# Kernel optimization log

Measured on AMD Instinct MI355X. Metric: run time of the kernel, lower is better.

Reference implementation:

```python
import jax, jax.numpy as jnp
import numpy as np

# Module hyperparameters (from init_kwargs)
DG = 8          # deformable_groups
KH = KW = 3     # kernel size
STRIDE = 1
PAD = 1
DIL = 1


def conv2d(x, w, b):
    # x: [B,C,H,W], w: [O,I,kh,kw] -> [B,O,Ho,Wo]
    y = jax.lax.conv_general_dilated(
        x, w, window_strides=(STRIDE, STRIDE),
        padding=[(PAD, PAD), (PAD, PAD)],
        rhs_dilation=(DIL, DIL),
        dimension_numbers=('NCHW', 'OIHW', 'NCHW'))
    return y + b[None, :, None, None]


def deform_conv2d(inp, offset, mask, w, b):
    # torchvision.ops.DeformConv2d (v2, with modulation mask), groups=1.
    # offset: [B, 2*DG*K, Ho, Wo] laid out as (dg, k, (dy,dx));
    # mask:   [B, DG*K, Ho, Wo] (already sigmoided).
    B, C, H, W = inp.shape
    Cout = w.shape[0]
    K = KH * KW
    Ho, Wo = offset.shape[2], offset.shape[3]
    Cg = C // DG

    off = offset.reshape(B, DG, K, 2, Ho, Wo)
    # base sampling grid per kernel tap
    ky = jnp.repeat(jnp.arange(KH) * DIL, KW)        # [K]
    kx = jnp.tile(jnp.arange(KW) * DIL, KH)          # [K]
    ybase = jnp.arange(Ho) * STRIDE - PAD            # [Ho]
    xbase = jnp.arange(Wo) * STRIDE - PAD            # [Wo]
    ys = off[:, :, :, 0] + (ky[:, None, None] + ybase[None, :, None])  # [B,DG,K,Ho,Wo]
    xs = off[:, :, :, 1] + (kx[:, None, None] + xbase[None, None, :])

    y0 = jnp.floor(ys)
    x0 = jnp.floor(xs)
    wy = (ys - y0)[:, :, None]   # [B,DG,1,K,Ho,Wo]
    wx = (xs - x0)[:, :, None]
    y0i = y0.astype(jnp.int32)
    x0i = x0.astype(jnp.int32)

    flat = inp.reshape(B, DG, Cg, H * W)

    def gather(yi, xi):
        valid = (yi >= 0) & (yi < H) & (xi >= 0) & (xi < W)        # [B,DG,K,Ho,Wo]
        idx = jnp.clip(yi, 0, H - 1) * W + jnp.clip(xi, 0, W - 1)
        idxf = idx.reshape(B, DG, -1)
        g = jax.vmap(jax.vmap(lambda f, i: jnp.take(f, i, axis=1)))(flat, idxf)
        g = g.reshape(B, DG, Cg, K, Ho, Wo)
        return g * valid[:, :, None].astype(inp.dtype)

    v00 = gather(y0i, x0i)
    v01 = gather(y0i, x0i + 1)
    v10 = gather(y0i + 1, x0i)
    v11 = gather(y0i + 1, x0i + 1)
    val = (v00 * (1 - wy) * (1 - wx) + v01 * (1 - wy) * wx
           + v10 * wy * (1 - wx) + v11 * wy * wx)
    val = val * mask.reshape(B, DG, 1, K, Ho, Wo)
    val = val.reshape(B, C, K, Ho, Wo)
    out = jnp.einsum('bckhw,ock->bohw', val, w.reshape(Cout, C, K))
    return out + b[None, :, None, None]


def setup_inputs() -> dict:
    key = jax.random.key(0)
    ks = jax.random.split(key, 8)
    B, C, Cf, Cout, H, W = 4, 64, 64, 64, 128, 128
    K = KH * KW
    inp = jax.random.normal(ks[0], (B, C, H, W), jnp.float32)
    feature = jax.random.normal(ks[1], (B, Cf, H, W), jnp.float32)
    # conv_offset / conv_mask params (small init so sampled offsets stay local)
    w_off = 0.05 * jax.random.normal(ks[2], (2 * DG * K, Cf, KH, KW), jnp.float32)
    b_off = jnp.zeros((2 * DG * K,), jnp.float32)
    w_mask = 0.05 * jax.random.normal(ks[3], (DG * K, Cf, KH, KW), jnp.float32)
    b_mask = jnp.zeros((DG * K,), jnp.float32)
    # deform conv params
    fan_in = C * KH * KW
    w_dcn = jax.random.normal(ks[4], (Cout, C, KH, KW), jnp.float32) / np.sqrt(fan_in)
    b_dcn = 0.01 * jax.random.normal(ks[5], (Cout,), jnp.float32)
    return {"input": inp, "feature": feature,
            "w_off": w_off, "b_off": b_off,
            "w_mask": w_mask, "b_mask": b_mask,
            "w_dcn": w_dcn, "b_dcn": b_dcn}


def reference(input, feature, w_off, b_off, w_mask, b_mask, w_dcn, b_dcn):
    offset = conv2d(feature, w_off, b_off)
    mask = jax.nn.sigmoid(conv2d(feature, w_mask, b_mask))
    return deform_conv2d(input, offset, mask, w_dcn, b_dcn)
```

## Files before the change

### kernel.cpp

```cpp
#include <hip/hip_runtime.h>
#include <hip/hip_bf16.h>

#define NB 4
#define CIN 64
#define COUT 64
#define HH 128
#define WW 128
#define HW (HH*WW)
#define C_OFF 144
#define C_OM 216
#define C_PAD 224
#define KTOT 576

typedef __attribute__((ext_vector_type(8))) short bf16x8;
typedef __attribute__((ext_vector_type(4))) float f32x4;
typedef __attribute__((ext_vector_type(8))) unsigned short uv8;

__device__ inline unsigned short f2bf(float f) {
    union { float f; unsigned u; } v; v.f = f;
    unsigned r = (v.u + 0x7FFF + ((v.u >> 16) & 1)) >> 16;
    return (unsigned short)r;
}

__device__ inline float bf2f(unsigned short h) {
    union { unsigned u; float f; } v; v.u = ((unsigned)h) << 16; return v.f;
}


__global__ __launch_bounds__(256) void transpose_wdcn(const float* __restrict__ w,
                                                      float* __restrict__ wT) {
    int idx = blockIdx.x * 256 + threadIdx.x;
    if (idx < KTOT * COUT) {
        int o = idx & 63, kk = idx >> 6;
        wT[idx] = w[o * KTOT + kk];
    }
}

__global__ __launch_bounds__(256) void to_nhwc_bf16_2(const float* __restrict__ f0,
                                                      unsigned short* __restrict__ o0,
                                                      const float* __restrict__ f1,
                                                      unsigned short* __restrict__ o1) {
    int t = blockIdx.x * 256 + threadIdx.x;
    const float* src;
    unsigned short* dst;
    int tt = t & 65535;
    int b = tt >> 14, yx = tt & 16383;
    if (t < 65536) { src = f0 + (size_t)b * CIN * HW + yx; dst = o0 + (size_t)tt * 64; }
    else           { src = f1 + (size_t)b * CIN * HW + yx; dst = o1 + (size_t)tt * 64; }
#pragma unroll
    for (int c8 = 0; c8 < 8; ++c8) {
        uv8 v;
#pragma unroll
        for (int j = 0; j < 8; ++j) v[j] = f2bf(src[(size_t)(c8 * 8 + j) * HW]);
        *(uv8*)(dst + c8 * 8) = v;
    }
}

__global__ __launch_bounds__(256) void prep_weights(const float* __restrict__ w_off,
                                                    const float* __restrict__ w_mask,
                                                    const float* __restrict__ w_dcn,
                                                    unsigned short* __restrict__ wB,
                                                    unsigned short* __restrict__ wTf2) {
    int idx = blockIdx.x * 256 + threadIdx.x;
    if (idx < C_PAD * KTOT) {
        int co = idx / KTOT, k = idx - co * KTOT;
        int t = k >> 6, ci = k & 63;
        float v = 0.f;
        if (co < C_OFF)      v = w_off[(size_t)co * KTOT + ci * 9 + t];
        else if (co < C_OM)  v = w_mask[(size_t)(co - C_OFF) * KTOT + ci * 9 + t];
        wB[idx] = f2bf(v);
    } else if (idx < C_PAD * KTOT + 72 * 64 * 8) {
        int j = idx - C_PAD * KTOT;
        int q = j >> 9;
        int co = (j >> 3) & 63;
        int r = j & 7;
        int k = q >> 3, dg = q & 7;
        wTf2[j] = f2bf(w_dcn[(size_t)co * KTOT + (dg * 8 + r) * 9 + k]);
    }
}


__global__ __launch_bounds__(256, 4) void dcn_fused(
    const unsigned short* __restrict__ fnhwc,
    const unsigned short* __restrict__ inb,
    const unsigned short* __restrict__ wB,
    const unsigned short* __restrict__ wTf2,
    const float* __restrict__ b_off, const float* __restrict__ b_mask,
    const float* __restrict__ b_dcn,
    float* __restrict__ out)
{
    __shared__ __align__(16) unsigned char smem[36864];
    unsigned short* Ash0  = (unsigned short*)smem;
    unsigned short* Ash1  = (unsigned short*)(smem + 4096);
    unsigned short* Bsh   = (unsigned short*)(smem + 8192);
    float* om_l           = (float*)smem;
    unsigned short* val_q = (unsigned short*)smem;

    int tid = threadIdx.x;
    int bid = blockIdx.x;
    int b   = bid >> 8;
    int hw0 = (bid & 255) << 6;
    int ho  = hw0 >> 7;
    int wo0 = hw0 & 127;

    int lane = tid & 63, wave = tid >> 6;
    int arow = lane & 15, g = lane >> 4;
    int h  = wave & 1;
    int ws = wave >> 1;

    f32x4 acc0[7], acc1[7];
#pragma unroll
    for (int n = 0; n < 7; ++n) {
        acc0[n] = (f32x4){0.f, 0.f, 0.f, 0.f};
        acc1[n] = (f32x4){0.f, 0.f, 0.f, 0.f};
    }

    int px_w = tid >> 3;
    int c8_w = tid & 7;
    const uv8 zero8 = (uv8){0, 0, 0, 0, 0, 0, 0, 0};

    for (int t = 0; t < 9; ++t) {
        int ky = t / 3, kx = t - ky * 3;
        int y = ho + ky - 1;
        bool yv = (unsigned)y < (unsigned)HH;
        __syncthreads();
#pragma unroll
        for (int pt = 0; pt < 2; ++pt) {
            int x = wo0 + pt * 32 + px_w + kx - 1;
            uv8 v = zero8;
            if (yv && (unsigned)x < (unsigned)WW)
                v = *(const uv8*)(fnhwc + ((size_t)((b * HH + y) * WW + x) << 6) + c8_w * 8);
            int off16 = (c8_w << 4) ^ ((px_w & 7) << 4);
            char* dst = (char*)(pt ? Ash1 : Ash0);
            *(uv8*)(dst + px_w * 128 + off16) = v;
        }
#pragma unroll
        for (int r = 0; r < 7; ++r) {
            int idx = r * 256 + tid;
            int co = idx >> 3, c8 = idx & 7;
            uv8 v = *(const uv8*)(wB + (size_t)co * KTOT + t * 64 + c8 * 8);
            *(uv8*)((char*)Bsh + co * 128 + ((c8 << 4) ^ ((co & 7) << 4))) = v;
        }
        __syncthreads();
#pragma unroll
        for (int half = 0; half < 2; ++half) {
            int px = h * 16 + arow;
            int kb = half * 64 + g * 16;
            bf16x8 a0 = *(const bf16x8*)((const char*)Ash0 + px * 128 + (kb ^ ((px & 7) << 4)));
            bf16x8 a1 = *(const bf16x8*)((const char*)Ash1 + px * 128 + (kb ^ ((px & 7) << 4)));
#pragma unroll
            for (int n = 0; n < 7; ++n) {
                int co = ws * 112 + n * 16 + arow;
                bf16x8 bf = *(const bf16x8*)((const char*)Bsh + co * 128 +
                                             (kb ^ ((co & 7) << 4)));
                acc0[n] = __builtin_amdgcn_mfma_f32_16x16x32_bf16(a0, bf, acc0[n], 0, 0, 0);
                acc1[n] = __builtin_amdgcn_mfma_f32_16x16x32_bf16(a1, bf, acc1[n], 0, 0, 0);
            }
        }
    }
    __syncthreads();

#pragma unroll
    for (int pt = 0; pt < 2; ++pt) {
        int hw0t = hw0 + pt * 32;
        int wo0t = wo0 + pt * 32;

#pragma unroll
        for (int n = 0; n < 7; ++n) {
            int co = ws * 112 + n * 16 + arow;
            if (co < C_OM) {
                float bias = (co < C_OFF) ? b_off[co] : b_mask[co - C_OFF];
                f32x4 av = pt ? acc1[n] : acc0[n];
#pragma unroll
                for (int j = 0; j < 4; ++j) {
                    float v = av[j] + bias;
                    if (co >= C_OFF) v = 1.f / (1.f + __expf(-v));
                    om_l[co * 33 + h * 16 + g * 4 + j] = v;
                }
            }
        }
        __syncthreads();

        int px = tid & 31;
        int dg = tid >> 5;

        float dy[9], dxv[9], mk[9];
#pragma unroll
        for (int k = 0; k < 9; ++k) {
            dy[k]  = om_l[(dg * 18 + 2 * k) * 33 + px];
            dxv[k] = om_l[(dg * 18 + 2 * k + 1) * 33 + px];
            mk[k]  = om_l[(C_OFF + dg * 9 + k) * 33 + px];
        }
        __syncthreads();

        const unsigned short* plane0 = inb + ((size_t)b * HW << 6) + dg * 8;
        float yb = (float)(ho - 1);
        float xb = (float)(wo0t + px - 1);

#pragma unroll
        for (int k = 0; k < 9; ++k) {
            float ys = dy[k] + yb + (float)(k / 3);
            float xs = dxv[k] + xb + (float)(k % 3);
            float y0f = floorf(ys), x0f = floorf(xs);
            float fy = ys - y0f, fx = xs - x0f;
            int y0 = (int)y0f, x0 = (int)x0f;
            bool yv0 = (unsigned)y0 < (unsigned)HH;
            bool yv1 = (unsigned)(y0 + 1) < (unsigned)HH;
            bool xv0 = (unsigned)x0 < (unsigned)WW;
            bool xv1 = (unsigned)(x0 + 1) < (unsigned)WW;
            const unsigned short* pp = plane0 + (y0 * WW + x0) * 64;
            uv8 c00 = zero8, c01 = zero8, c10 = zero8, c11 = zero8;
            if (yv0 && xv0) c00 = *(const uv8*)(pp);
            if (yv0 && xv1) c01 = *(const uv8*)(pp + 64);
            if (yv1 && xv0) c10 = *(const uv8*)(pp + 64 * WW);
            if (yv1 && xv1) c11 = *(const uv8*)(pp + 64 * WW + 64);
            uv8 r;
#pragma unroll
            for (int j = 0; j < 8; ++j) {
                float v00 = bf2f(c00[j]), v01 = bf2f(c01[j]);
                float v10 = bf2f(c10[j]), v11 = bf2f(c11[j]);
                float top = v00 + (v01 - v00) * fx;
                float bot = v10 + (v11 - v10) * fx;
                float v = top + (bot - top) * fy;
                r[j] = f2bf(v * mk[k]);
            }
            *(uv8*)(val_q + (k * 8 + dg) * 256 + px * 8) = r;
        }
        __syncthreads();

        int nh = wave >> 1;

        f32x4 dacc[2];
        dacc[0] = dacc[1] = (f32x4){0.f, 0.f, 0.f, 0.f};
#pragma unroll
        for (int s = 0; s < 18; ++s) {
            int q = s * 4 + g;
            bf16x8 a = *(const bf16x8*)(val_q + q * 256 + (h * 16 + arow) * 8);
#pragma unroll
            for (int n = 0; n < 2; ++n) {
                int co = nh * 32 + n * 16 + arow;
                bf16x8 bfr = *(const bf16x8*)(wTf2 + ((size_t)q * 64 + co) * 8);
                dacc[n] = __builtin_amdgcn_mfma_f32_16x16x32_bf16(a, bfr, dacc[n], 0, 0, 0);
            }
        }

#pragma unroll
        for (int n = 0; n < 2; ++n) {
            int co = nh * 32 + n * 16 + arow;
            float bias = b_dcn[co];
            f32x4 r;
#pragma unroll
            for (int j = 0; j < 4; ++j) r[j] = dacc[n][j] + bias;
            *(f32x4*)(out + (size_t)b * COUT * HW + (size_t)co * HW + hw0t + h * 16 + g * 4) = r;
        }
        __syncthreads();
    }
}


__global__ __launch_bounds__(256) void conv_om_kernel(
    const float* __restrict__ feature,
    const float* __restrict__ w_off, const float* __restrict__ b_off,
    const float* __restrict__ w_mask, const float* __restrict__ b_mask,
    float* __restrict__ om)
{
    int tid = threadIdx.x;
    int p = blockIdx.x * 256 + tid;
    int cg = blockIdx.y;
    int b  = p >> 14;
    int hw = p & (HW - 1);
    int ho = hw >> 7;
    int wo = hw & 127;
    int co0 = cg * 4;

    float acc[4];
    const float* wb[4];
#pragma unroll
    for (int j = 0; j < 4; ++j) {
        int co = co0 + j;
        if (co < C_OFF) { acc[j] = b_off[co];          wb[j] = w_off  + (size_t)co * 576; }
        else            { acc[j] = b_mask[co - C_OFF]; wb[j] = w_mask + (size_t)(co - C_OFF) * 576; }
    }
    const float* fb = feature + (size_t)b * CIN * HW;
    for (int ci = 0; ci < CIN; ++ci) {
        const float* fp = fb + ci * HW;
#pragma unroll
        for (int ky = 0; ky < 3; ++ky) {
            int y = ho + ky - 1;
            bool yvb = (unsigned)y < (unsigned)HH;
#pragma unroll
            for (int kx = 0; kx < 3; ++kx) {
                int x = wo + kx - 1;
                float v = (yvb && (unsigned)x < (unsigned)WW) ? fp[y * WW + x] : 0.f;
                int wi = ci * 9 + ky * 3 + kx;
#pragma unroll
                for (int j = 0; j < 4; ++j) acc[j] += v * wb[j][wi];
            }
        }
    }
    size_t obase = (size_t)b * C_OM * HW + hw;
#pragma unroll
    for (int j = 0; j < 4; ++j) {
        int co = co0 + j;
        float v = acc[j];
        if (co >= C_OFF) v = 1.f / (1.f + __expf(-v));
        om[obase + (size_t)co * HW] = v;
    }
}

__global__ __launch_bounds__(256) void dcn_kernel(
    const float* __restrict__ input,
    const float* __restrict__ om,
    const float* __restrict__ wT,
    const float* __restrict__ b_dcn,
    float* __restrict__ out)
{
    __shared__ float om_l[C_OM * 16];
    __shared__ float val_l[KTOT * 16];

    int tid  = threadIdx.x;
    int tile = blockIdx.x;
    int b    = tile >> 10;
    int hw0  = (tile & 1023) << 4;
    int ho   = hw0 >> 7;
    int wo0  = hw0 & 127;

    const float* omg = om + (size_t)b * C_OM * HW + hw0;
    for (int i = tid; i < C_OM * 16; i += 256) {
        int ch = i >> 4, px = i & 15;
        om_l[i] = omg[(size_t)ch * HW + px];
    }
    __syncthreads();

    for (int pair = tid; pair < 1024; pair += 256) {
        int px = pair & 15, c = pair >> 4;
        int dg = c >> 3;
        const float* plane = input + (size_t)(b * CIN + c) * HW;
        float yb = (float)(ho - 1);
        float xb = (float)(wo0 + px - 1);
#pragma unroll
        for (int k = 0; k < 9; ++k) {
            float dyv = om_l[(dg * 18 + 2 * k) * 16 + px];
            float dxv = om_l[(dg * 18 + 2 * k + 1) * 16 + px];
            float m  = om_l[(C_OFF + dg * 9 + k) * 16 + px];
            float ys = dyv + yb + (float)(k / 3);
            float xs = dxv + xb + (float)(k % 3);
            float y0f = floorf(ys), x0f = floorf(xs);
            float wy = ys - y0f, wx = xs - x0f;
            int y0 = (int)y0f, x0 = (int)x0f;
            bool yv0 = (unsigned)y0 < (unsigned)HH;
            bool yv1 = (unsigned)(y0 + 1) < (unsigned)HH;
            bool xv0 = (unsigned)x0 < (unsigned)WW;
            bool xv1 = (unsigned)(x0 + 1) < (unsigned)WW;
            const float* r0 = plane + y0 * WW + x0;
            float v00 = (yv0 && xv0) ? r0[0]      : 0.f;
            float v01 = (yv0 && xv1) ? r0[1]      : 0.f;
            float v10 = (yv1 && xv0) ? r0[WW]     : 0.f;
            float v11 = (yv1 && xv1) ? r0[WW + 1] : 0.f;
            float top = v00 + (v01 - v00) * wx;
            float bot = v10 + (v11 - v10) * wx;
            float v = top + (bot - top) * wy;
            val_l[(c * 9 + k) * 16 + px] = v * m;
        }
    }
    __syncthreads();

    int o2 = tid & 31;
    int ph = tid >> 5;
    int o0 = o2 * 2, px0 = ph * 2;
    float a00 = b_dcn[o0],     a01 = b_dcn[o0];
    float a10 = b_dcn[o0 + 1], a11 = b_dcn[o0 + 1];
    for (int kk = 0; kk < KTOT; ++kk) {
        float2 wv = *reinterpret_cast<const float2*>(wT + kk * 64 + o0);
        float va = val_l[kk * 16 + px0];
        float vb = val_l[kk * 16 + px0 + 1];
        a00 += wv.x * va; a01 += wv.x * vb;
        a10 += wv.y * va; a11 += wv.y * vb;
    }
    float* ob = out + (size_t)b * COUT * HW + hw0;
    ob[(size_t)o0 * HW + px0]           = a00;
    ob[(size_t)o0 * HW + px0 + 1]       = a01;
    ob[(size_t)(o0 + 1) * HW + px0]     = a10;
    ob[(size_t)(o0 + 1) * HW + px0 + 1] = a11;
}

extern "C" void kernel_launch(void* const* d_in, const int* in_sizes, int n_in,
                              void* d_out, int out_size, void* d_ws, size_t ws_size,
                              hipStream_t stream) {
    const float* input   = (const float*)d_in[0];
    const float* feature = (const float*)d_in[1];
    const float* w_off   = (const float*)d_in[2];
    const float* b_off   = (const float*)d_in[3];
    const float* w_mask  = (const float*)d_in[4];
    const float* b_mask  = (const float*)d_in[5];
    const float* w_dcn   = (const float*)d_in[6];
    const float* b_dcn   = (const float*)d_in[7];
    float* out = (float*)d_out;

    unsigned short* fnhwc = (unsigned short*)d_ws;
    unsigned short* wBp   = fnhwc + (size_t)NB * HW * CIN;
    unsigned short* wTfp  = wBp + (size_t)C_PAD * KTOT;
    unsigned short* inb   = wTfp + 72 * 64 * 8;
    size_t need_full = (size_t)((char*)(inb + (size_t)NB * HW * CIN) - (char*)d_ws);
    size_t need_fb = ((size_t)NB * C_OM * HW + KTOT * COUT) * sizeof(float);

    if (ws_size >= need_full) {
        to_nhwc_bf16_2<<<NB * HW * 2 / 256, 256, 0, stream>>>(feature, fnhwc, input, inb);
        prep_weights<<<(C_PAD * KTOT + 72 * 64 * 8 + 255) / 256, 256, 0, stream>>>(
            w_off, w_mask, w_dcn, wBp, wTfp);
        dcn_fused<<<NB * HW / 64, 256, 0, stream>>>(fnhwc, inb, wBp, wTfp,
                                                    b_off, b_mask, b_dcn, out);
    } else if (ws_size >= need_fb) {
        float* om = (float*)d_ws;
        float* wT = om + (size_t)NB * C_OM * HW;
        transpose_wdcn<<<(KTOT * COUT + 255) / 256, 256, 0, stream>>>(w_dcn, wT);
        dim3 cgrid(NB * HW / 256, 54);
        conv_om_kernel<<<cgrid, 256, 0, stream>>>(feature, w_off, b_off, w_mask, b_mask, om);
        dcn_kernel<<<NB * HW / 16, 256, 0, stream>>>(input, om, wT, b_dcn, out);
    }
}
```

Before: 88.51 us.

## Prefetch next tap's A and B tiles into registers during MFMA compute

Restructures the offset/mask conv tap loop so the global loads for the next kernel tap are issued into registers before the current tap's MFMA work, then written to shared memory after a barrier. The aim is to hide global memory latency behind matrix compute instead of stalling at each tap. In exchange it raises register pressure by about nine extra 16-byte vectors per thread, which may reduce occupancy.

```diff
diff --git a/kernel.cpp b/kernel.cpp
--- a/kernel.cpp
+++ b/kernel.cpp
@@ -117,31 +117,52 @@
 
     int px_w = tid >> 3;
     int c8_w = tid & 7;
+    int off16A = (c8_w << 4) ^ ((px_w & 7) << 4);
     const uv8 zero8 = (uv8){0, 0, 0, 0, 0, 0, 0, 0};
 
-    for (int t = 0; t < 9; ++t) {
-        int ky = t / 3, kx = t - ky * 3;
-        int y = ho + ky - 1;
+    {
+        int y = ho - 1;
         bool yv = (unsigned)y < (unsigned)HH;
-        __syncthreads();
 #pragma unroll
         for (int pt = 0; pt < 2; ++pt) {
-            int x = wo0 + pt * 32 + px_w + kx - 1;
+            int x = wo0 + pt * 32 + px_w - 1;
             uv8 v = zero8;
             if (yv && (unsigned)x < (unsigned)WW)
                 v = *(const uv8*)(fnhwc + ((size_t)((b * HH + y) * WW + x) << 6) + c8_w * 8);
-            int off16 = (c8_w << 4) ^ ((px_w & 7) << 4);
             char* dst = (char*)(pt ? Ash1 : Ash0);
-            *(uv8*)(dst + px_w * 128 + off16) = v;
+            *(uv8*)(dst + px_w * 128 + off16A) = v;
         }
 #pragma unroll
         for (int r = 0; r < 7; ++r) {
             int idx = r * 256 + tid;
             int co = idx >> 3, c8 = idx & 7;
-            uv8 v = *(const uv8*)(wB + (size_t)co * KTOT + t * 64 + c8 * 8);
+            uv8 v = *(const uv8*)(wB + (size_t)co * KTOT + c8 * 8);
             *(uv8*)((char*)Bsh + co * 128 + ((c8 << 4) ^ ((co & 7) << 4))) = v;
         }
-        __syncthreads();
+    }
+    __syncthreads();
+
+    for (int t = 0; t < 9; ++t) {
+        uv8 nA0 = zero8, nA1 = zero8, nB[7];
+        if (t < 8) {
+            int nt = t + 1;
+            int ky = nt / 3, kx = nt - ky * 3;
+            int y = ho + ky - 1;
+            bool yv = (unsigned)y < (unsigned)HH;
+            int x0_ = wo0 + px_w + kx - 1;
+            if (yv && (unsigned)x0_ < (unsigned)WW)
+                nA0 = *(const uv8*)(fnhwc + ((size_t)((b * HH + y) * WW + x0_) << 6) + c8_w * 8);
+            int x1_ = x0_ + 32;
+            if (yv && (unsigned)x1_ < (unsigned)WW)
+                nA1 = *(const uv8*)(fnhwc + ((size_t)((b * HH + y) * WW + x1_) << 6) + c8_w * 8);
+#pragma unroll
+            for (int r = 0; r < 7; ++r) {
+                int idx = r * 256 + tid;
+                int co = idx >> 3, c8 = idx & 7;
+                nB[r] = *(const uv8*)(wB + (size_t)co * KTOT + nt * 64 + c8 * 8);
+            }
+        }
+
 #pragma unroll
         for (int half = 0; half < 2; ++half) {
             int px = h * 16 + arow;
@@ -157,8 +178,20 @@
                 acc1[n] = __builtin_amdgcn_mfma_f32_16x16x32_bf16(a1, bf, acc1[n], 0, 0, 0);
             }
         }
-    }
-    __syncthreads();
+        __syncthreads();
+
+        if (t < 8) {
+            *(uv8*)((char*)Ash0 + px_w * 128 + off16A) = nA0;
+            *(uv8*)((char*)Ash1 + px_w * 128 + off16A) = nA1;
+#pragma unroll
+            for (int r = 0; r < 7; ++r) {
+                int idx = r * 256 + tid;
+                int co = idx >> 3, c8 = idx & 7;
+                *(uv8*)((char*)Bsh + co * 128 + ((c8 << 4) ^ ((co & 7) << 4))) = nB[r];
+            }
+            __syncthreads();
+        }
+    }
 
 #pragma unroll
     for (int pt = 0; pt < 2; ++pt) {
```

Result: slower. 103.0 us (+16.3%).
